# Performance work log

Hardware: AMD Instinct MI355X
Metric: run time of the kernel (lower is better)

## Reference

```python
import math
import jax, jax.numpy as jnp
import numpy as np

B, K, D, N = 64, 16384, 128, 500000
T = 0.07          # nce_t
MOM = 0.5         # nce_momentum (EMA for memory bank update)


def setup_inputs() -> dict:
    key = jax.random.key(0)
    k0, k1, k2, k3, k4, k5 = jax.random.split(key, 6)
    stdv = 1.0 / math.sqrt(D / 3.0)
    memory_l = jax.random.uniform(k0, (N, D), dtype=jnp.float32) * (2 * stdv) - stdv
    memory_ab = jax.random.uniform(k1, (N, D), dtype=jnp.float32) * (2 * stdv) - stdv
    l = jax.random.normal(k2, (B, D), dtype=jnp.float32)
    ab = jax.random.normal(k3, (B, D), dtype=jnp.float32)
    # unique positive indices so the index_copy_ scatter is well-defined
    y = jax.random.permutation(k4, N)[:B].astype(jnp.int64)
    idx = jax.random.randint(k5, (B, K + 1), 0, N, dtype=jnp.int64)
    idx = idx.at[:, 0].set(y)  # slot 0 holds the positive sample, as in torch code
    return {"l": l, "ab": ab, "memory_l": memory_l, "memory_ab": memory_ab,
            "y": y, "idx": idx}


def reference(l, ab, memory_l, memory_ab, y, idx):
    # gather -> batched dot-product scoring (use_softmax=True branch: just /T)
    weight_l = memory_l[idx]            # (B, K+1, D)  gather from bank
    out_ab = jnp.einsum('bkd,bd->bk', weight_l, ab)[..., None] / T   # (B, K+1, 1)
    weight_ab = memory_ab[idx]          # (B, K+1, D)
    out_l = jnp.einsum('bkd,bd->bk', weight_ab, l)[..., None] / T    # (B, K+1, 1)

    # momentum EMA + L2-normalize + scatter update of the memory banks (no-grad in torch)
    def ema_update(mem, feat):
        pos = mem[y] * MOM + feat * (1.0 - MOM)                       # (B, D)
        pos = pos / jnp.sqrt(jnp.sum(pos * pos, axis=1, keepdims=True))
        return mem.at[y].set(pos)

    new_memory_l = ema_update(memory_l, l)
    new_memory_ab = ema_update(memory_ab, ab)
    return out_l, out_ab, new_memory_l, new_memory_ab
```

## Files before the change

### kernel.cpp

```cpp
#include <hip/hip_runtime.h>
#include <math.h>

#define B_    64
#define KP1   16385
#define D_    128
#define NROW  500000
#define INV_T (1.0f / 0.07f)
#define MOM_  0.5f

#define BK_    (B_ * KP1)
#define NE4B   (NROW * (D_ / 4))
#define CHUNKSZ 2048
#define NCHUNK  245
#define PADROWS (NCHUNK * CHUNKSZ)

#define NBLK   2048
#define NGRP   (NBLK * 8)

#define WS_COUNTS   0
#define WS_PARTIAL  (WS_COUNTS  + PADROWS * 4)
#define WS_BSUM     (WS_PARTIAL + PADROWS * 4)
#define WS_BSCAN    (WS_BSUM    + 256 * 4)
#define WS_RANK     (WS_BSCAN   + 256 * 4)
#define WS_ENTRIES  (WS_RANK    + BK_ * 4)

__device__ __forceinline__ float dot4(const float4 r, const float4 f) {
    return r.x * f.x + r.y * f.y + r.z * f.z + r.w * f.w;
}

__global__ __launch_bounds__(256)
void hist_kernel(const int* __restrict__ idx, int* __restrict__ counts,
                 int* __restrict__ rank) {
    for (unsigned u = blockIdx.x * 256u + threadIdx.x; u < (unsigned)BK_;
         u += gridDim.x * 256u) {
        const int r = idx[u];
        rank[u] = atomicAdd(&counts[r], 1);
    }
}

__global__ __launch_bounds__(256)
void scan1_kernel(const int* __restrict__ counts, int* __restrict__ partial,
                  int* __restrict__ bsum) {
    __shared__ int tsum[256];
    const int tid  = threadIdx.x;
    const int base = blockIdx.x * CHUNKSZ + tid * 8;

    int c[8], pre[8], run = 0;
    #pragma unroll
    for (int i = 0; i < 8; ++i) c[i] = counts[base + i];
    #pragma unroll
    for (int i = 0; i < 8; ++i) { pre[i] = run; run += c[i]; }

    tsum[tid] = run;
    __syncthreads();
    for (int off = 1; off < 256; off <<= 1) {
        const int add = (tid >= off) ? tsum[tid - off] : 0;
        __syncthreads();
        tsum[tid] += add;
        __syncthreads();
    }
    const int toff = tsum[tid] - run;
    #pragma unroll
    for (int i = 0; i < 8; ++i) partial[base + i] = toff + pre[i];
    if (tid == 255) bsum[blockIdx.x] = tsum[255];
}

__global__ __launch_bounds__(256)
void scan2_kernel(const int* __restrict__ bsum, int* __restrict__ bscan) {
    __shared__ int tsum[256];
    const int tid = threadIdx.x;
    const int v = (tid < NCHUNK) ? bsum[tid] : 0;
    tsum[tid] = v;
    __syncthreads();
    for (int off = 1; off < 256; off <<= 1) {
        const int add = (tid >= off) ? tsum[tid - off] : 0;
        __syncthreads();
        tsum[tid] += add;
        __syncthreads();
    }
    bscan[tid] = tsum[tid] - v;
}

__global__ __launch_bounds__(256)
void scatter_kernel(const int* __restrict__ idx, const int* __restrict__ rank,
                    const int* __restrict__ partial, const int* __restrict__ bscan,
                    int* __restrict__ entries) {
    for (unsigned u = blockIdx.x * 256u + threadIdx.x; u < (unsigned)BK_;
         u += gridDim.x * 256u) {
        const int r = idx[u];
        const int pos = partial[r] + bscan[r >> 11] + rank[u];
        entries[pos] = (int)u;
    }
}

__global__ __launch_bounds__(256)
void stream_kernel(const float* __restrict__ l,
                   const float* __restrict__ ab,
                   const float* __restrict__ mem_l,
                   const float* __restrict__ mem_ab,
                   const int* __restrict__ partial,
                   const int* __restrict__ bscan,
                   const int* __restrict__ entries,
                   float* __restrict__ out,
                   float* __restrict__ out_mem_l,
                   float* __restrict__ out_mem_ab) {
    const int glane = threadIdx.x & 31;
    const unsigned g = (blockIdx.x << 3) + (threadIdx.x >> 5);

    for (unsigned r = g; r < (unsigned)NROW; r += NGRP) {
        const float4 rl = ((const float4*)(mem_l  + (size_t)r * D_))[glane];
        const float4 ra = ((const float4*)(mem_ab + (size_t)r * D_))[glane];
        ((float4*)(out_mem_l  + (size_t)r * D_))[glane] = rl;
        ((float4*)(out_mem_ab + (size_t)r * D_))[glane] = ra;

        const int o0 = partial[r]     + bscan[r >> 11];
        const int o1 = partial[r + 1] + bscan[(r + 1) >> 11];

        for (int e = o0; e < o1; ++e) {
            const unsigned u = (unsigned)entries[e];
            const unsigned b = u / KP1;
            const float4 fl = ((const float4*)(l  + (size_t)b * D_))[glane];
            const float4 fa = ((const float4*)(ab + (size_t)b * D_))[glane];
            float sl = dot4(ra, fl);
            float sa = dot4(rl, fa);
            #pragma unroll
            for (int m = 16; m >= 1; m >>= 1) {
                sl += __shfl_xor(sl, m);
                sa += __shfl_xor(sa, m);
            }
            if (glane == 0) out[u]       = sl * INV_T;
            if (glane == 1) out[BK_ + u] = sa * INV_T;
        }
    }
}

__global__ __launch_bounds__(128)
void ema_update_kernel(const float* __restrict__ l,
                       const float* __restrict__ ab,
                       const float* __restrict__ mem_l,
                       const float* __restrict__ mem_ab,
                       const int* __restrict__ y,
                       float* __restrict__ out_mem_l,
                       float* __restrict__ out_mem_ab) {
    const int b    = blockIdx.x;
    const int wave = threadIdx.x >> 6;
    const int lane = threadIdx.x & 63;
    const int yb   = y[b];

    const float* mem  = wave ? mem_ab     : mem_l;
    const float* feat = wave ? ab         : l;
    float*       om   = wave ? out_mem_ab : out_mem_l;

    const float2 m2 = ((const float2*)(mem  + (size_t)yb * D_))[lane];
    const float2 f2 = ((const float2*)(feat + (size_t)b  * D_))[lane];

    float px = m2.x * MOM_ + f2.x * (1.0f - MOM_);
    float py = m2.y * MOM_ + f2.y * (1.0f - MOM_);
    float ss = px * px + py * py;
    #pragma unroll
    for (int m = 32; m >= 1; m >>= 1) ss += __shfl_xor(ss, m);
    const float rn = 1.0f / sqrtf(ss);

    ((float2*)(om + (size_t)yb * D_))[lane] = make_float2(px * rn, py * rn);
}

extern "C" void kernel_launch(void* const* d_in, const int* in_sizes, int n_in,
                              void* d_out, int out_size, void* d_ws, size_t ws_size,
                              hipStream_t stream) {
    const float* l      = (const float*)d_in[0];
    const float* ab     = (const float*)d_in[1];
    const float* mem_l  = (const float*)d_in[2];
    const float* mem_ab = (const float*)d_in[3];
    const int*   y      = (const int*)d_in[4];
    const int*   idx    = (const int*)d_in[5];
    float* out = (float*)d_out;

    float* out_mem_l  = out + (size_t)(2 * BK_);
    float* out_mem_ab = out_mem_l + (size_t)NROW * D_;

    char* ws = (char*)d_ws;
    int* counts  = (int*)(ws + WS_COUNTS);
    int* partial = (int*)(ws + WS_PARTIAL);
    int* bsum    = (int*)(ws + WS_BSUM);
    int* bscan   = (int*)(ws + WS_BSCAN);
    int* rank    = (int*)(ws + WS_RANK);
    int* entries = (int*)(ws + WS_ENTRIES);

    hipMemsetAsync(counts, 0, (size_t)PADROWS * 4, stream);
    hist_kernel   <<<2048, 256, 0, stream>>>(idx, counts, rank);
    scan1_kernel  <<<NCHUNK, 256, 0, stream>>>(counts, partial, bsum);
    scan2_kernel  <<<1, 256, 0, stream>>>(bsum, bscan);
    scatter_kernel<<<2048, 256, 0, stream>>>(idx, rank, partial, bscan, entries);
    stream_kernel <<<NBLK, 256, 0, stream>>>(l, ab, mem_l, mem_ab,
                                             partial, bscan, entries,
                                             out, out_mem_l, out_mem_ab);
    ema_update_kernel<<<B_, 128, 0, stream>>>(l, ab, mem_l, mem_ab, y,
                                              out_mem_l, out_mem_ab);
}
```

Before: 349.8 us.

## Flatten sorted entries into balanced quads and interleave bank copy with gathers

Entries are now (row, u) pairs in row-sorted order, produced by an atomic cursor in the scatter kernel instead of a stored rank array. The stream kernel processes exactly four entries per wave-group per step, giving even load balance and more loads in flight. The full memory-bank copy is split into flat nontemporal vector copies interleaved with the gather/dot work. This removes the per-row loop and its uneven trip counts, but rows are now re-read from the bank per entry rather than reused, which relies on sorted order for cache hits. The atomic cursor also makes the order within a row nondeterministic.

```diff
diff --git a/kernel.cpp b/kernel.cpp
--- a/kernel.cpp
+++ b/kernel.cpp
@@ -10,32 +10,35 @@
 
 #define BK_    (B_ * KP1)
 #define NE4B   (NROW * (D_ / 4))
+#define NBLK   2048
+#define NTHR   (NBLK * 256)
+#define NGRP   (NBLK * 8)
+#define NQUADE (BK_ / 4)
+#define NSTEP  16
+#define REMG   (NQUADE - NSTEP * NGRP)
+#define CPITER 31
+
 #define CHUNKSZ 2048
 #define NCHUNK  245
 #define PADROWS (NCHUNK * CHUNKSZ)
-
-#define NBLK   2048
-#define NGRP   (NBLK * 8)
 
 #define WS_COUNTS   0
 #define WS_PARTIAL  (WS_COUNTS  + PADROWS * 4)
 #define WS_BSUM     (WS_PARTIAL + PADROWS * 4)
 #define WS_BSCAN    (WS_BSUM    + 256 * 4)
-#define WS_RANK     (WS_BSCAN   + 256 * 4)
-#define WS_ENTRIES  (WS_RANK    + BK_ * 4)
+#define WS_ENTRIES  (WS_BSCAN   + 256 * 4)
+
+typedef float vfloat4 __attribute__((ext_vector_type(4)));
 
 __device__ __forceinline__ float dot4(const float4 r, const float4 f) {
     return r.x * f.x + r.y * f.y + r.z * f.z + r.w * f.w;
 }
 
 __global__ __launch_bounds__(256)
-void hist_kernel(const int* __restrict__ idx, int* __restrict__ counts,
-                 int* __restrict__ rank) {
+void hist_kernel(const int* __restrict__ idx, int* __restrict__ counts) {
     for (unsigned u = blockIdx.x * 256u + threadIdx.x; u < (unsigned)BK_;
-         u += gridDim.x * 256u) {
-        const int r = idx[u];
-        rank[u] = atomicAdd(&counts[r], 1);
-    }
+         u += gridDim.x * 256u)
+        atomicAdd(&counts[idx[u]], 1);
 }
 
 __global__ __launch_bounds__(256)
@@ -82,14 +85,79 @@
 }
 
 __global__ __launch_bounds__(256)
-void scatter_kernel(const int* __restrict__ idx, const int* __restrict__ rank,
-                    const int* __restrict__ partial, const int* __restrict__ bscan,
-                    int* __restrict__ entries) {
+void scatter_kernel(const int* __restrict__ idx, int* __restrict__ cursor,
+                    const int* __restrict__ bscan, int2* __restrict__ entries) {
     for (unsigned u = blockIdx.x * 256u + threadIdx.x; u < (unsigned)BK_;
          u += gridDim.x * 256u) {
         const int r = idx[u];
-        const int pos = partial[r] + bscan[r >> 11] + rank[u];
-        entries[pos] = (int)u;
+        const int pos = atomicAdd(&cursor[r], 1) + bscan[r >> 11];
+        entries[pos] = make_int2(r, (int)u);
+    }
+}
+
+__device__ __forceinline__ void copy_iter(const vfloat4* __restrict__ src,
+                                          vfloat4* __restrict__ dst,
+                                          int c, unsigned tid) {
+    if (c < CPITER) {
+        const size_t e = (size_t)c * NTHR + tid;
+        if (e < (size_t)NE4B)
+            __builtin_nontemporal_store(src[e], dst + e);
+    }
+}
+
+__device__ __forceinline__ void entry_quad(
+        unsigned q, int glane,
+        const float* __restrict__ l, const float* __restrict__ ab,
+        const float* __restrict__ mem_l, const float* __restrict__ mem_ab,
+        const int2* __restrict__ entries, float* __restrict__ out) {
+    const int4 w0 = ((const int4*)(entries + 4u * q))[0];
+    const int4 w1 = ((const int4*)(entries + 4u * q))[1];
+    const int r0 = w0.x, u0 = w0.y, r1 = w0.z, u1 = w0.w;
+    const int r2 = w1.x, u2 = w1.y, r3 = w1.z, u3 = w1.w;
+
+    const unsigned b0 = (unsigned)u0 / KP1, b1 = (unsigned)u1 / KP1;
+    const unsigned b2 = (unsigned)u2 / KP1, b3 = (unsigned)u3 / KP1;
+
+    const float4 a0 = ((const float4*)(mem_ab + (size_t)r0 * D_))[glane];
+    const float4 m0 = ((const float4*)(mem_l  + (size_t)r0 * D_))[glane];
+    const float4 a1 = ((const float4*)(mem_ab + (size_t)r1 * D_))[glane];
+    const float4 m1 = ((const float4*)(mem_l  + (size_t)r1 * D_))[glane];
+    const float4 a2 = ((const float4*)(mem_ab + (size_t)r2 * D_))[glane];
+    const float4 m2 = ((const float4*)(mem_l  + (size_t)r2 * D_))[glane];
+    const float4 a3 = ((const float4*)(mem_ab + (size_t)r3 * D_))[glane];
+    const float4 m3 = ((const float4*)(mem_l  + (size_t)r3 * D_))[glane];
+
+    const float4 fl0 = ((const float4*)(l  + (size_t)b0 * D_))[glane];
+    const float4 fa0 = ((const float4*)(ab + (size_t)b0 * D_))[glane];
+    const float4 fl1 = ((const float4*)(l  + (size_t)b1 * D_))[glane];
+    const float4 fa1 = ((const float4*)(ab + (size_t)b1 * D_))[glane];
+    const float4 fl2 = ((const float4*)(l  + (size_t)b2 * D_))[glane];
+    const float4 fa2 = ((const float4*)(ab + (size_t)b2 * D_))[glane];
+    const float4 fl3 = ((const float4*)(l  + (size_t)b3 * D_))[glane];
+    const float4 fa3 = ((const float4*)(ab + (size_t)b3 * D_))[glane];
+
+    float sl0 = dot4(a0, fl0), sa0 = dot4(m0, fa0);
+    float sl1 = dot4(a1, fl1), sa1 = dot4(m1, fa1);
+    float sl2 = dot4(a2, fl2), sa2 = dot4(m2, fa2);
+    float sl3 = dot4(a3, fl3), sa3 = dot4(m3, fa3);
+
+    #pragma unroll
+    for (int m = 16; m >= 1; m >>= 1) {
+        sl0 += __shfl_xor(sl0, m);  sa0 += __shfl_xor(sa0, m);
+        sl1 += __shfl_xor(sl1, m);  sa1 += __shfl_xor(sa1, m);
+        sl2 += __shfl_xor(sl2, m);  sa2 += __shfl_xor(sa2, m);
+        sl3 += __shfl_xor(sl3, m);  sa3 += __shfl_xor(sa3, m);
+    }
+    if (glane == 0) {
+        __builtin_nontemporal_store(sl0 * INV_T, out + u0);
+        __builtin_nontemporal_store(sl1 * INV_T, out + u1);
+        __builtin_nontemporal_store(sl2 * INV_T, out + u2);
+        __builtin_nontemporal_store(sl3 * INV_T, out + u3);
+    } else if (glane == 1) {
+        __builtin_nontemporal_store(sa0 * INV_T, out + BK_ + u0);
+        __builtin_nontemporal_store(sa1 * INV_T, out + BK_ + u1);
+        __builtin_nontemporal_store(sa2 * INV_T, out + BK_ + u2);
+        __builtin_nontemporal_store(sa3 * INV_T, out + BK_ + u3);
     }
 }
 
@@ -98,40 +166,30 @@
                    const float* __restrict__ ab,
                    const float* __restrict__ mem_l,
                    const float* __restrict__ mem_ab,
-                   const int* __restrict__ partial,
-                   const int* __restrict__ bscan,
-                   const int* __restrict__ entries,
+                   const int2* __restrict__ entries,
                    float* __restrict__ out,
                    float* __restrict__ out_mem_l,
                    float* __restrict__ out_mem_ab) {
-    const int glane = threadIdx.x & 31;
-    const unsigned g = (blockIdx.x << 3) + (threadIdx.x >> 5);
-
-    for (unsigned r = g; r < (unsigned)NROW; r += NGRP) {
-        const float4 rl = ((const float4*)(mem_l  + (size_t)r * D_))[glane];
-        const float4 ra = ((const float4*)(mem_ab + (size_t)r * D_))[glane];
-        ((float4*)(out_mem_l  + (size_t)r * D_))[glane] = rl;
-        ((float4*)(out_mem_ab + (size_t)r * D_))[glane] = ra;
-
-        const int o0 = partial[r]     + bscan[r >> 11];
-        const int o1 = partial[r + 1] + bscan[(r + 1) >> 11];
-
-        for (int e = o0; e < o1; ++e) {
-            const unsigned u = (unsigned)entries[e];
-            const unsigned b = u / KP1;
-            const float4 fl = ((const float4*)(l  + (size_t)b * D_))[glane];
-            const float4 fa = ((const float4*)(ab + (size_t)b * D_))[glane];
-            float sl = dot4(ra, fl);
-            float sa = dot4(rl, fa);
-            #pragma unroll
-            for (int m = 16; m >= 1; m >>= 1) {
-                sl += __shfl_xor(sl, m);
-                sa += __shfl_xor(sa, m);
-            }
-            if (glane == 0) out[u]       = sl * INV_T;
-            if (glane == 1) out[BK_ + u] = sa * INV_T;
-        }
-    }
+    const unsigned tid   = blockIdx.x * 256u + threadIdx.x;
+    const int      glane = threadIdx.x & 31;
+    const unsigned g     = (blockIdx.x << 3) + (threadIdx.x >> 5);
+
+    const vfloat4* srcL = (const vfloat4*)mem_l;
+    const vfloat4* srcA = (const vfloat4*)mem_ab;
+    vfloat4* dstL = (vfloat4*)out_mem_l;
+    vfloat4* dstA = (vfloat4*)out_mem_ab;
+
+    for (int j = 0; j < NSTEP; ++j) {
+        copy_iter(srcL, dstL, 2 * j,     tid);
+        copy_iter(srcA, dstA, 2 * j,     tid);
+        copy_iter(srcL, dstL, 2 * j + 1, tid);
+        copy_iter(srcA, dstA, 2 * j + 1, tid);
+        entry_quad(g + (unsigned)j * NGRP, glane,
+                   l, ab, mem_l, mem_ab, entries, out);
+    }
+    if (g < REMG)
+        entry_quad((unsigned)NSTEP * NGRP + g, glane,
+                   l, ab, mem_l, mem_ab, entries, out);
 }
 
 __global__ __launch_bounds__(128)
@@ -179,20 +237,18 @@
     float* out_mem_ab = out_mem_l + (size_t)NROW * D_;
 
     char* ws = (char*)d_ws;
-    int* counts  = (int*)(ws + WS_COUNTS);
-    int* partial = (int*)(ws + WS_PARTIAL);
-    int* bsum    = (int*)(ws + WS_BSUM);
-    int* bscan   = (int*)(ws + WS_BSCAN);
-    int* rank    = (int*)(ws + WS_RANK);
-    int* entries = (int*)(ws + WS_ENTRIES);
+    int*  counts  = (int*)(ws + WS_COUNTS);
+    int*  partial = (int*)(ws + WS_PARTIAL);
+    int*  bsum    = (int*)(ws + WS_BSUM);
+    int*  bscan   = (int*)(ws + WS_BSCAN);
+    int2* entries = (int2*)(ws + WS_ENTRIES);
 
     hipMemsetAsync(counts, 0, (size_t)PADROWS * 4, stream);
-    hist_kernel   <<<2048, 256, 0, stream>>>(idx, counts, rank);
+    hist_kernel   <<<2048, 256, 0, stream>>>(idx, counts);
     scan1_kernel  <<<NCHUNK, 256, 0, stream>>>(counts, partial, bsum);
     scan2_kernel  <<<1, 256, 0, stream>>>(bsum, bscan);
-    scatter_kernel<<<2048, 256, 0, stream>>>(idx, rank, partial, bscan, entries);
-    stream_kernel <<<NBLK, 256, 0, stream>>>(l, ab, mem_l, mem_ab,
-                                             partial, bscan, entries,
+    scatter_kernel<<<2048, 256, 0, stream>>>(idx, partial, bscan, entries);
+    stream_kernel <<<NBLK, 256, 0, stream>>>(l, ab, mem_l, mem_ab, entries,
                                              out, out_mem_l, out_mem_ab);
     ema_update_kernel<<<B_, 128, 0, stream>>>(l, ab, mem_l, mem_ab, y,
                                               out_mem_l, out_mem_ab);
```

After: 470.8 us. +34.6%, slower.
